# Optimization experiments

Measured on AMD Instinct MI355X. Metric: run time of the kernel, lower is better.

The kernel has to match this reference:

```python
import jax, jax.numpy as jnp
import numpy as np

N_MEL = 80; ENC = 512; ARNN = 1024; DRNN = 1024; PRE = 256
ADIM = 128; NFILT = 32; KS = 31
B = 16; T_ENC = 128; T_DEC = 128
NEG = -1e30  # stand-in for -inf mask value


def _lstm_cell(x, h, c, wih, whh, bih, bhh):
    # PyTorch LSTMCell gate order: i, f, g, o
    gates = x @ wih.T + h @ whh.T + bih + bhh
    i, f, g, o = jnp.split(gates, 4, axis=-1)
    c = jax.nn.sigmoid(f) * c + jax.nn.sigmoid(i) * jnp.tanh(g)
    h = jax.nn.sigmoid(o) * jnp.tanh(c)
    return h, c


def _forward(memory, mels, memory_lengths, prenet_w1, prenet_w2,
             arnn_wih, arnn_whh, arnn_bih, arnn_bhh,
             query_w, memory_w, v_w, loc_conv_w, loc_dense_w,
             drnn_wih, drnn_whh, drnn_bih, drnn_bhh,
             proj_w, proj_b, gate_w, gate_b):
    bsz, t_enc, enc = memory.shape
    t_dec = mels.shape[2]
    valid = jnp.arange(t_enc)[None, :] < memory_lengths[:, None]  # [B,T_enc]
    proc_mem = memory @ memory_w.T  # [B,T_enc,ADIM], precomputed once

    # parse_decoder_inputs + go frame: use go frame + teacher frames 0..T-2
    teacher = jnp.transpose(mels, (2, 0, 1))  # [T_dec,B,n_mel]
    go = jnp.zeros((1, bsz, mels.shape[1]), mels.dtype)
    dec_in = jnp.concatenate([go, teacher], axis=0)[:t_dec]
    # Prenet (dropout is p=0.0 in source, so omitted)
    x = jax.nn.relu(dec_in @ prenet_w1.T)
    x = jax.nn.relu(x @ prenet_w2.T)  # [T_dec,B,PRE]

    pad = (KS - 1) // 2

    def step(carry, x_t):
        attn_h, attn_c, dec_h, dec_c, aw, awc, ctx = carry
        # attention RNN
        cell_in = jnp.concatenate([x_t, ctx], axis=-1)
        attn_h2, attn_c2 = _lstm_cell(cell_in, attn_h, attn_c,
                                      arnn_wih, arnn_whh, arnn_bih, arnn_bhh)
        # location-sensitive attention
        aw_cat = jnp.stack([aw, awc], axis=1)  # [B,2,T_enc]
        loc = jax.lax.conv_general_dilated(
            aw_cat, loc_conv_w, (1,), [(pad, pad)],
            dimension_numbers=('NCH', 'OIH', 'NCH'))  # [B,NFILT,T_enc]
        loc = jnp.einsum('bft,af->bta', loc, loc_dense_w)  # [B,T_enc,ADIM]
        pq = attn_h2 @ query_w.T  # [B,ADIM]
        e = jnp.tanh(pq[:, None, :] + loc + proc_mem) @ v_w[0]  # [B,T_enc]
        e = jnp.where(valid, e, NEG)
        aw2 = jax.nn.softmax(e, axis=1)
        ctx2 = jnp.einsum('bt,bte->be', aw2, memory)  # [B,ENC]
        awc2 = awc + aw2
        # decoder RNN
        dec_in2 = jnp.concatenate([attn_h2, ctx2], axis=-1)
        dec_h2, dec_c2 = _lstm_cell(dec_in2, dec_h, dec_c,
                                    drnn_wih, drnn_whh, drnn_bih, drnn_bhh)
        hc = jnp.concatenate([dec_h2, ctx2], axis=-1)
        mel = hc @ proj_w.T + proj_b      # [B,n_mel]
        gate = hc @ gate_w.T + gate_b     # [B,1]
        new_carry = (attn_h2, attn_c2, dec_h2, dec_c2, aw2, awc2, ctx2)
        return new_carry, (mel, gate[:, 0], aw2)

    z = lambda *s: jnp.zeros(s, memory.dtype)
    carry0 = (z(bsz, ARNN), z(bsz, ARNN), z(bsz, DRNN), z(bsz, DRNN),
              z(bsz, t_enc), z(bsz, t_enc), z(bsz, enc))
    _, (mels_out, gates, aligns) = jax.lax.scan(step, carry0, x)
    mel_outputs = jnp.transpose(mels_out, (1, 2, 0))   # [B,n_mel,T_dec]
    gate_outputs = jnp.transpose(gates, (1, 0))        # [B,T_dec]
    alignments = jnp.transpose(aligns, (1, 0, 2))      # [B,T_dec,T_enc]
    return mel_outputs, gate_outputs, alignments


def setup_inputs() -> dict:
    key = jax.random.key(0)
    ks = jax.random.split(key, 24)

    def g(i, shape):
        fan_in = shape[-1] if len(shape) <= 2 else int(np.prod(shape[1:]))
        return jax.random.normal(ks[i], shape, jnp.float32) / np.float32(np.sqrt(fan_in))

    return {
        'memory': jax.random.normal(ks[0], (B, T_ENC, ENC), jnp.float32),
        'mels': jax.random.normal(ks[1], (B, N_MEL, T_DEC), jnp.float32),
        'memory_lengths': jax.random.randint(ks[2], (B,), T_ENC // 2, T_ENC + 1),
        'prenet_w1': g(3, (PRE, N_MEL)),
        'prenet_w2': g(4, (PRE, PRE)),
        'arnn_wih': g(5, (4 * ARNN, PRE + ENC)),
        'arnn_whh': g(6, (4 * ARNN, ARNN)),
        'arnn_bih': g(7, (4 * ARNN,)),
        'arnn_bhh': g(8, (4 * ARNN,)),
        'query_w': g(9, (ADIM, ARNN)),
        'memory_w': g(10, (ADIM, ENC)),
        'v_w': g(11, (1, ADIM)),
        'loc_conv_w': g(12, (NFILT, 2, KS)),
        'loc_dense_w': g(13, (ADIM, NFILT)),
        'drnn_wih': g(14, (4 * DRNN, ARNN + ENC)),
        'drnn_whh': g(15, (4 * DRNN, DRNN)),
        'drnn_bih': g(16, (4 * DRNN,)),
        'drnn_bhh': g(17, (4 * DRNN,)),
        'proj_w': g(18, (N_MEL, DRNN + ENC)),
        'proj_b': g(19, (N_MEL,)),
        'gate_w': g(20, (1, DRNN + ENC)),
        'gate_b': g(21, (1,)),
    }


def reference(memory, mels, memory_lengths, prenet_w1, prenet_w2,
              arnn_wih, arnn_whh, arnn_bih, arnn_bhh,
              query_w, memory_w, v_w, loc_conv_w, loc_dense_w,
              drnn_wih, drnn_whh, drnn_bih, drnn_bhh,
              proj_w, proj_b, gate_w, gate_b):
    return _forward(memory, mels, memory_lengths, prenet_w1, prenet_w2,
                    arnn_wih, arnn_whh, arnn_bih, arnn_bhh,
                    query_w, memory_w, v_w, loc_conv_w, loc_dense_w,
                    drnn_wih, drnn_whh, drnn_bih, drnn_bhh,
                    proj_w, proj_b, gate_w, gate_b)
```

## Files before the change

kernel.cpp:

```cpp
#include <hip/hip_runtime.h>
#include <hip/hip_cooperative_groups.h>

namespace cg = cooperative_groups;

#define N_MEL 80
#define ENC   512
#define ARNN  1024
#define PRE   256
#define ADIM  128
#define NFILT 32
#define KS    31
#define BSZ   16
#define TENC  128
#define TDEC  128

#define OFF_XA     0u
#define OFF_X      8388608u
#define OFF_H1     8912896u
#define OFF_DECIN  9437184u
#define OFF_PM     9601024u
#define OFF_ATTNH  9863168u
#define OFF_DECH   9895936u
#define OFF_CTX    9928704u
#define OFF_CTR    9945088u
#define STATE_FLOATS 82496

typedef float vf4 __attribute__((ext_vector_type(4)));

__device__ __forceinline__ float sigmf(float x) { return 1.0f / (1.0f + __expf(-x)); }
__device__ __forceinline__ float tanhfast(float x) { return 1.0f - 2.0f / (__expf(2.0f * x) + 1.0f); }
__device__ __forceinline__ float dot4(const float4& w, const vf4& x) {
    return w.x * x.x + w.y * x.y + w.z * x.z + w.w * x.w;
}
__device__ __forceinline__ float dot4f(const float4& w, const float4& x) {
    return w.x * x.x + w.y * x.y + w.z * x.z + w.w * x.w;
}

__device__ __forceinline__ vf4 vload4(const float* p) { return *(const volatile vf4*)p; }
__device__ __forceinline__ float vloadf(const float* p) { return *(const volatile float*)p; }
__device__ __forceinline__ void vstoref(float* p, float v) { *(volatile float*)p = v; }

__device__ __forceinline__ void wait_ge(unsigned* p, unsigned tgt) {
    while (__hip_atomic_load(p, __ATOMIC_RELAXED, __HIP_MEMORY_SCOPE_AGENT) < tgt)
        __builtin_amdgcn_s_sleep(1);
    asm volatile("" ::: "memory");
}


__global__ void __launch_bounds__(1024) build_decin(const float* __restrict__ mels,
                                                    float* __restrict__ decin) {
    int idx = blockIdx.x * 1024 + threadIdx.x;
    if (idx >= 128 * 16 * 80) return;
    int t = idx / 1280, r = idx % 1280;
    int b = r / 80, m = r % 80;
    decin[idx] = (t == 0) ? 0.f : mels[b * (80 * 128) + m * 128 + (t - 1)];
}

__global__ void __launch_bounds__(256) gemm_kernel(
    const float* __restrict__ A, int lda,
    const float* __restrict__ B, int ldb,
    float* __restrict__ C, int ldc,
    int M, int N, int K,
    const float* __restrict__ bias1, const float* __restrict__ bias2, int relu) {
    __shared__ float As[16][68];
    __shared__ float Bs[16][68];
    int tid = threadIdx.x;
    int tn = tid & 15, tm = tid >> 4;
    int m0 = blockIdx.y * 64, n0 = blockIdx.x * 64;
    float acc[4][4] = {};
    for (int k0 = 0; k0 < K; k0 += 16) {
        for (int idx = tid; idx < 1024; idx += 256) {
            int mm = idx >> 4, kk = idx & 15;
            int kg = k0 + kk;
            As[kk][mm] = (kg < K) ? A[(size_t)(m0 + mm) * lda + kg] : 0.f;
            Bs[kk][mm] = (kg < K) ? B[(size_t)(n0 + mm) * ldb + kg] : 0.f;
        }
        __syncthreads();
#pragma unroll
        for (int kk = 0; kk < 16; kk++) {
            float av[4], bv[4];
#pragma unroll
            for (int i = 0; i < 4; i++) { av[i] = As[kk][tm * 4 + i]; bv[i] = Bs[kk][tn * 4 + i]; }
#pragma unroll
            for (int i = 0; i < 4; i++)
#pragma unroll
                for (int j = 0; j < 4; j++) acc[i][j] += av[i] * bv[j];
        }
        __syncthreads();
    }
    for (int i = 0; i < 4; i++) {
        int m = m0 + tm * 4 + i;
        for (int j = 0; j < 4; j++) {
            int n = n0 + tn * 4 + j;
            float v = acc[i][j];
            if (bias1) v += bias1[n];
            if (bias2) v += bias2[n];
            if (relu) v = fmaxf(v, 0.f);
            C[(size_t)m * ldc + n] = v;
        }
    }
}


struct DecArgs {
    const float* memory;
    const int* memlen;
    const float* arnn_wih;
    const float* arnn_whh;
    const float* drnn_wih;
    const float* drnn_whh;
    const float* drnn_bih;
    const float* drnn_bhh;
    const float* query_w;
    const float* v_w;
    const float* conv_w;
    const float* dense_w;
    const float* proj_w;
    const float* proj_b;
    const float* gate_w;
    const float* gate_b;
    float* ws;
    float* out;
};

__global__ void __launch_bounds__(512, 2) decoder_main(DecArgs A) {
    cg::grid_group grid = cg::this_grid();
    const int tid = threadIdx.x;
    const int wv = tid >> 6;
    const int l = tid & 63;
    const int blk = blockIdx.x;
    const int u = wv & 3;
    const int kq = wv >> 2;
    const int jj = blk * 4 + u;
    const int col = kq * 256 + l * 4;
    float* ws = A.ws;
    unsigned* ctrA = (unsigned*)(ws + OFF_CTR);
    unsigned* ctrB = (unsigned*)(ws + OFF_CTR + 32);
    const int grp = blk >> 4;
    unsigned* subA = (unsigned*)(ws + OFF_CTR + 64 + grp * 32);

    __shared__ float s_pm[128 * 132];
    __shared__ float s_loc[128 * 33];
    __shared__ float s_dw[128 * 33];
    __shared__ float s_cw[1984];
    __shared__ float s_ah[1024];
    __shared__ float s_ep[512];
    __shared__ float s_part[8][64];
    __shared__ float s_pp[8][64];
    __shared__ float s_pq[128];
    __shared__ float s_aw2[128];
    __shared__ float s_awl[128];
    __shared__ float s_awcl[128];
    __shared__ float s_attnc[64];
    __shared__ float s_decc[64];
    __shared__ float s_db[16];
    __shared__ float s_vw[128];
    __shared__ float s_red[2];

    {
        int g = blk * 512 + tid;
        if (g < STATE_FLOATS) ws[OFF_ATTNH + g] = 0.f;
    }
    if (tid < 128) { s_awl[tid] = 0.f; s_awcl[tid] = 0.f; }
    if (tid < 64) { s_attnc[tid] = 0.f; s_decc[tid] = 0.f; }
    if (tid < 16) {
        int uu = tid >> 2, gg = tid & 3;
        s_db[tid] = A.drnn_bih[gg * 1024 + blk * 4 + uu] + A.drnn_bhh[gg * 1024 + blk * 4 + uu];
    }
    if (tid < 128) s_vw[tid] = A.v_w[tid];
    for (int idx = tid; idx < 4096; idx += 512) {
        int a = idx >> 5, f = idx & 31;
        s_dw[a * 33 + f] = A.dense_w[idx];
    }
    if (blk < 16) {
        for (int idx = tid; idx < 16384; idx += 512) {
            int tt = idx >> 7, a = idx & 127;
            s_pm[tt * 132 + a] = ws[OFF_PM + (blk * 128 + tt) * 128 + a];
        }
        for (int idx = tid; idx < 1984; idx += 512) s_cw[idx] = A.conv_w[idx];
    }
    const int ml = (blk < 16) ? A.memlen[blk] : 0;

    float4 wA[12];
    {
#pragma unroll
        for (int g = 0; g < 4; g++)
            wA[g] = *reinterpret_cast<const float4*>(
                A.arnn_wih + (size_t)(g * 1024 + jj) * 768 + 256 + col);
#pragma unroll
        for (int ch = 1; ch < 3; ch++)
#pragma unroll
            for (int g = 0; g < 4; g++)
                wA[ch * 4 + g] = *reinterpret_cast<const float4*>(
                    A.arnn_whh + (size_t)(g * 1024 + jj) * 1024 + (ch - 1) * 512 + col);
    }
    float4 wD[20];
    {
#pragma unroll
        for (int ch = 0; ch < 3; ch++)
#pragma unroll
            for (int g = 0; g < 4; g++)
                wD[ch * 4 + g] = *reinterpret_cast<const float4*>(
                    A.drnn_wih + (size_t)(g * 1024 + jj) * 1536 + ch * 512 + col);
#pragma unroll
        for (int ch = 3; ch < 5; ch++)
#pragma unroll
            for (int g = 0; g < 4; g++)
                wD[ch * 4 + g] = *reinterpret_cast<const float4*>(
                    A.drnn_whh + (size_t)(g * 1024 + jj) * 1024 + (ch - 3) * 512 + col);
    }
    __syncthreads();
    grid.sync();

    auto reduce4 = [&](float p0, float p1, float p2, float p3) -> float {
        float a01 = (l & 1) ? p1 : p0;
        float b01 = (l & 1) ? p0 : p1;
        a01 += __shfl_xor(b01, 1);
        float a23 = (l & 1) ? p3 : p2;
        float b23 = (l & 1) ? p2 : p3;
        a23 += __shfl_xor(b23, 1);
        float k_ = (l & 2) ? a23 : a01;
        float s_ = (l & 2) ? a01 : a23;
        k_ += __shfl_xor(s_, 2);
        k_ += __shfl_xor(k_, 4);
        k_ += __shfl_xor(k_, 8);
        k_ += __shfl_xor(k_, 16);
        k_ += __shfl_xor(k_, 32);
        return k_;
    };

    auto attn_stage = [&](int t, int wpar, int rpar) {
        const float* hb = ws + OFF_ATTNH + rpar * 16384;
        const float* cb = ws + OFF_CTX + rpar * 8192;
        float xa0 = 0.f, xa1 = 0.f, xa2 = 0.f, xa3 = 0.f;
        if (tid < 64) {
            int eb = tid & 15, eu = tid >> 4;
            const float* xa = ws + OFF_XA + (size_t)(t * 16 + eb) * 4096 + (blk * 4 + eu);
            xa0 = xa[0]; xa1 = xa[1024]; xa2 = xa[2048]; xa3 = xa[3072];
        }
#pragma unroll 4
        for (int b = 0; b < 16; b++) {
            vf4 x0 = vload4(cb + b * 512 + col);
            vf4 x1 = vload4(hb + b * 1024 + col);
            vf4 x2 = vload4(hb + b * 1024 + 512 + col);
            float p0 = dot4(wA[0], x0) + dot4(wA[4], x1) + dot4(wA[8], x2);
            float p1 = dot4(wA[1], x0) + dot4(wA[5], x1) + dot4(wA[9], x2);
            float p2 = dot4(wA[2], x0) + dot4(wA[6], x1) + dot4(wA[10], x2);
            float p3 = dot4(wA[3], x0) + dot4(wA[7], x1) + dot4(wA[11], x2);
            float r = reduce4(p0, p1, p2, p3);
            if (l < 4) s_part[wv][b * 4 + l] = r;
        }
        __syncthreads();
        if (tid < 64) {
            int eu = tid >> 4, eb = tid & 15;
            float G0 = s_part[eu][eb * 4 + 0] + s_part[eu + 4][eb * 4 + 0] + xa0;
            float G1 = s_part[eu][eb * 4 + 1] + s_part[eu + 4][eb * 4 + 1] + xa1;
            float G2 = s_part[eu][eb * 4 + 2] + s_part[eu + 4][eb * 4 + 2] + xa2;
            float G3 = s_part[eu][eb * 4 + 3] + s_part[eu + 4][eb * 4 + 3] + xa3;
            float ig = sigmf(G0), fg = sigmf(G1), gg = tanhfast(G2), og = sigmf(G3);
            float c = fg * s_attnc[tid] + ig * gg;
            s_attnc[tid] = c;
            vstoref(ws + OFF_ATTNH + wpar * 16384 + eb * 1024 + blk * 4 + eu, og * tanhfast(c));
        }
    };

    auto dec_partial = [&](int wpar, int rpar) {
        const float* hb = ws + OFF_ATTNH + wpar * 16384;
        const float* db = ws + OFF_DECH + rpar * 16384;
#pragma unroll 2
        for (int b = 0; b < 16; b++) {
            vf4 x0 = vload4(hb + b * 1024 + col);
            vf4 x1 = vload4(hb + b * 1024 + 512 + col);
            vf4 x3 = vload4(db + b * 1024 + col);
            vf4 x4 = vload4(db + b * 1024 + 512 + col);
            float p0 = dot4(wD[0], x0) + dot4(wD[4], x1) + dot4(wD[12], x3) + dot4(wD[16], x4);
            float p1 = dot4(wD[1], x0) + dot4(wD[5], x1) + dot4(wD[13], x3) + dot4(wD[17], x4);
            float p2 = dot4(wD[2], x0) + dot4(wD[6], x1) + dot4(wD[14], x3) + dot4(wD[18], x4);
            float p3 = dot4(wD[3], x0) + dot4(wD[7], x1) + dot4(wD[15], x3) + dot4(wD[19], x4);
            float r = reduce4(p0, p1, p2, p3);
            if (l < 4) s_pp[wv][b * 4 + l] = r;
        }
    };

    auto dec_tail = [&](int wpar) {
        const float* cb = ws + OFF_CTX + wpar * 8192;
#pragma unroll 4
        for (int b = 0; b < 16; b++) {
            vf4 x2 = vload4(cb + b * 512 + col);
            float p0 = dot4(wD[8], x2);
            float p1 = dot4(wD[9], x2);
            float p2 = dot4(wD[10], x2);
            float p3 = dot4(wD[11], x2);
            float r = reduce4(p0, p1, p2, p3);
            if (l < 4) s_part[wv][b * 4 + l] = r;
        }
        __syncthreads();
        if (tid < 64) {
            int eu = tid >> 4, eb = tid & 15;
            float G0 = s_part[eu][eb * 4 + 0] + s_part[eu + 4][eb * 4 + 0]
                     + s_pp[eu][eb * 4 + 0] + s_pp[eu + 4][eb * 4 + 0] + s_db[eu * 4 + 0];
            float G1 = s_part[eu][eb * 4 + 1] + s_part[eu + 4][eb * 4 + 1]
                     + s_pp[eu][eb * 4 + 1] + s_pp[eu + 4][eb * 4 + 1] + s_db[eu * 4 + 1];
            float G2 = s_part[eu][eb * 4 + 2] + s_part[eu + 4][eb * 4 + 2]
                     + s_pp[eu][eb * 4 + 2] + s_pp[eu + 4][eb * 4 + 2] + s_db[eu * 4 + 2];
            float G3 = s_part[eu][eb * 4 + 3] + s_part[eu + 4][eb * 4 + 3]
                     + s_pp[eu][eb * 4 + 3] + s_pp[eu + 4][eb * 4 + 3] + s_db[eu * 4 + 3];
            float ig = sigmf(G0), fg = sigmf(G1), gg = tanhfast(G2), og = sigmf(G3);
            float c = fg * s_decc[tid] + ig * gg;
            s_decc[tid] = c;
            vstoref(ws + OFF_DECH + wpar * 16384 + eb * 1024 + blk * 4 + eu, og * tanhfast(c));
        }
        __syncthreads();
    };

    auto attention = [&](int t, int wpar) {
        const int b = blk;
        s_ah[tid] = vloadf(ws + OFF_ATTNH + wpar * 16384 + b * 1024 + tid);
        s_ah[tid + 512] = vloadf(ws + OFF_ATTNH + wpar * 16384 + b * 1024 + 512 + tid);
        for (int idx = tid; idx < 4096; idx += 512) {
            int f = idx >> 7, tt = idx & 127;
            const float* w0 = s_cw + f * 62;
            float s = 0.f;
#pragma unroll
            for (int k = 0; k < 31; k++) {
                int j = tt + k - 15;
                if (j >= 0 && j < 128) s += w0[k] * s_awl[j] + w0[31 + k] * s_awcl[j];
            }
            s_loc[tt * 33 + f] = s;
        }
        __syncthreads();
#pragma unroll 4
        for (int ii = 0; ii < 16; ii++) {
            int a = wv * 16 + ii;
            const float* qw = A.query_w + a * 1024;
            float s = 0.f;
#pragma unroll
            for (int q = 0; q < 4; q++) {
                int k = q * 256 + l * 4;
                float4 h4 = *reinterpret_cast<const float4*>(&s_ah[k]);
                float4 w4 = *reinterpret_cast<const float4*>(&qw[k]);
                s += dot4f(w4, h4);
            }
#pragma unroll
            for (int off = 1; off < 64; off <<= 1) s += __shfl_xor(s, off);
            if (l == 0) s_pq[a] = s;
        }
        __syncthreads();
        {
            int tt = tid >> 2, sl = tid & 3;
            float part = 0.f;
            for (int i = 0; i < 32; i++) {
                int a = i * 4 + sl;
                float lp = 0.f;
#pragma unroll
                for (int f = 0; f < 32; f++) lp += s_loc[tt * 33 + f] * s_dw[a * 33 + f];
                float arg = s_pq[a] + lp + s_pm[tt * 132 + a];
                part += s_vw[a] * tanhfast(arg);
            }
            s_ep[tid] = part;
        }
        __syncthreads();
        if (tid < 128) {
            float s = s_ep[tid * 4] + s_ep[tid * 4 + 1] + s_ep[tid * 4 + 2] + s_ep[tid * 4 + 3];
            s_aw2[tid] = (tid >= ml) ? 0.f : __expf(s);
        }
        __syncthreads();
        if (wv == 0) {
            float s = s_aw2[l] + s_aw2[l + 64];
#pragma unroll
            for (int off = 1; off < 64; off <<= 1) s += __shfl_xor(s, off);
            if (l == 0) s_red[0] = 1.f / s;
        }
        __syncthreads();
        if (tid < 128) {
            float val = s_aw2[tid] * s_red[0];
            s_aw2[tid] = val;
            s_awl[tid] = val;
            s_awcl[tid] += val;
            A.out[165888 + b * 16384 + t * 128 + tid] = val;
        }
        __syncthreads();
        {
            const float* mb = A.memory + (size_t)b * 65536 + tid;
            float acc = 0.f;
#pragma unroll 8
            for (int tt2 = 0; tt2 < 128; tt2++) acc += s_aw2[tt2] * mb[tt2 * 512];
            vstoref(ws + OFF_CTX + wpar * 8192 + b * 512 + tid, acc);
        }
    };

    auto eout = [&](int tdone) {
        int widx = (blk - 16) * 8 + wv;
        if (widx >= 1296) return;
        int ppar = tdone & 1;
        int b; const float* wrow; float bias; float* dst;
        if (widx < 1280) {
            b = widx / 80; int m = widx % 80;
            wrow = A.proj_w + m * 1536; bias = A.proj_b[m];
            dst = A.out + (size_t)(b * 80 + m) * 128 + tdone;
        } else {
            b = widx - 1280;
            wrow = A.gate_w; bias = A.gate_b[0];
            dst = A.out + 163840 + b * 128 + tdone;
        }
        const float* h1p = ws + OFF_DECH + ppar * 16384 + b * 1024;
        const float* c1p = ws + OFF_CTX + ppar * 8192 + b * 512;
        float s = 0.f;
#pragma unroll
        for (int q = 0; q < 6; q++) {
            int k = q * 256 + l * 4;
            float4 w4 = *reinterpret_cast<const float4*>(&wrow[k]);
            vf4 h4;
            if (k < 1024) h4 = vload4(h1p + k);
            else h4 = vload4(c1p + k - 1024);
            s += dot4(w4, h4);
        }
#pragma unroll
        for (int off = 1; off < 64; off <<= 1) s += __shfl_xor(s, off);
        if (l == 0) *dst = s + bias;
    };

    for (int t = 0; t < 128; t++) {
        int wpar = t & 1, rpar = wpar ^ 1;
        attn_stage(t, wpar, rpar);
        __syncthreads();
        if (tid == 0) {
            asm volatile("s_waitcnt vmcnt(0)" ::: "memory");
            unsigned old = __hip_atomic_fetch_add(subA, 1u, __ATOMIC_RELAXED,
                                                  __HIP_MEMORY_SCOPE_AGENT);
            if (old == 16u * (unsigned)(t + 1) - 1u)
                __hip_atomic_fetch_add(ctrA, 1u, __ATOMIC_RELAXED,
                                       __HIP_MEMORY_SCOPE_AGENT);
        }
        if (blk < 16) {
            if (tid == 0) wait_ge(ctrA, 16u * (unsigned)(t + 1));
            __syncthreads();
            attention(t, wpar);
            __syncthreads();
            if (tid == 0) {
                asm volatile("s_waitcnt vmcnt(0)" ::: "memory");
                __hip_atomic_fetch_add(ctrB, 1u, __ATOMIC_RELAXED,
                                       __HIP_MEMORY_SCOPE_AGENT);
            }
            dec_partial(wpar, rpar);
            if (tid == 0) wait_ge(ctrB, 16u * (unsigned)(t + 1));
            __syncthreads();
            dec_tail(wpar);
        } else {
            if (tid == 0) wait_ge(ctrA, 16u * (unsigned)(t + 1));
            __syncthreads();
            if (t >= 1) eout(t - 1);
            dec_partial(wpar, rpar);
            if (tid == 0) wait_ge(ctrB, 16u * (unsigned)(t + 1));
            __syncthreads();
            dec_tail(wpar);
        }
    }
    if (tid == 0) {
        asm volatile("s_waitcnt vmcnt(0)" ::: "memory");
        unsigned old = __hip_atomic_fetch_add(subA, 1u, __ATOMIC_RELAXED,
                                              __HIP_MEMORY_SCOPE_AGENT);
        if (old == 16u * 129u - 1u)
            __hip_atomic_fetch_add(ctrA, 1u, __ATOMIC_RELAXED, __HIP_MEMORY_SCOPE_AGENT);
    }
    if (blk >= 16) {
        if (tid == 0) wait_ge(ctrA, 16u * 129u);
        __syncthreads();
        eout(127);
    }
}


extern "C" void kernel_launch(void* const* d_in, const int* in_sizes, int n_in,
                              void* d_out, int out_size, void* d_ws, size_t ws_size,
                              hipStream_t stream) {
    (void)in_sizes; (void)n_in; (void)out_size; (void)ws_size;
    const float* memory    = (const float*)d_in[0];
    const float* mels      = (const float*)d_in[1];
    const int*   memlen    = (const int*)d_in[2];
    const float* prenet_w1 = (const float*)d_in[3];
    const float* prenet_w2 = (const float*)d_in[4];
    const float* arnn_wih  = (const float*)d_in[5];
    const float* arnn_whh  = (const float*)d_in[6];
    const float* arnn_bih  = (const float*)d_in[7];
    const float* arnn_bhh  = (const float*)d_in[8];
    const float* query_w   = (const float*)d_in[9];
    const float* memory_w  = (const float*)d_in[10];
    const float* v_w       = (const float*)d_in[11];
    const float* conv_w    = (const float*)d_in[12];
    const float* dense_w   = (const float*)d_in[13];
    const float* drnn_wih  = (const float*)d_in[14];
    const float* drnn_whh  = (const float*)d_in[15];
    const float* drnn_bih  = (const float*)d_in[16];
    const float* drnn_bhh  = (const float*)d_in[17];
    const float* proj_w    = (const float*)d_in[18];
    const float* proj_b    = (const float*)d_in[19];
    const float* gate_w    = (const float*)d_in[20];
    const float* gate_b    = (const float*)d_in[21];
    float* ws = (float*)d_ws;
    float* out = (float*)d_out;

    build_decin<<<dim3(160), dim3(1024), 0, stream>>>(mels, ws + OFF_DECIN);
    gemm_kernel<<<dim3(4, 32), dim3(256), 0, stream>>>(ws + OFF_DECIN, 80, prenet_w1, 80,
                                                       ws + OFF_H1, 256, 2048, 256, 80,
                                                       nullptr, nullptr, 1);
    gemm_kernel<<<dim3(4, 32), dim3(256), 0, stream>>>(ws + OFF_H1, 256, prenet_w2, 256,
                                                       ws + OFF_X, 256, 2048, 256, 256,
                                                       nullptr, nullptr, 1);
    gemm_kernel<<<dim3(64, 32), dim3(256), 0, stream>>>(ws + OFF_X, 256, arnn_wih, 768,
                                                        ws + OFF_XA, 4096, 2048, 4096, 256,
                                                        arnn_bih, arnn_bhh, 0);
    gemm_kernel<<<dim3(2, 32), dim3(256), 0, stream>>>(memory, 512, memory_w, 512,
                                                       ws + OFF_PM, 128, 2048, 128, 512,
                                                       nullptr, nullptr, 0);

    DecArgs a;
    a.memory = memory; a.memlen = memlen;
    a.arnn_wih = arnn_wih; a.arnn_whh = arnn_whh;
    a.drnn_wih = drnn_wih; a.drnn_whh = drnn_whh;
    a.drnn_bih = drnn_bih; a.drnn_bhh = drnn_bhh;
    a.query_w = query_w; a.v_w = v_w;
    a.conv_w = conv_w; a.dense_w = dense_w;
    a.proj_w = proj_w; a.proj_b = proj_b;
    a.gate_w = gate_w; a.gate_b = gate_b;
    a.ws = ws; a.out = out;
    void* kargs[] = { &a };
    hipLaunchCooperativeKernel((const void*)decoder_main, dim3(256), dim3(512),
                               kargs, 0, stream);
}
```

Baseline: 12.00 ms.

## Hierarchical barrier broadcast with LDS spin and overlapped location conv

Attention blocks now post barrier completion to per-group broadcast flags, so the other blocks spin on a group-local global word instead of all polling the same counters. Inside each block, the non-leader waves spin on an LDS flag while doing dummy FMA work, which keeps them busy rather than idling at the barrier. The location convolution is moved ahead of the attention-stage wait so it overlaps the global barrier. This adds more synchronization state, and the busy spinning could compete with the leader thread or affect clock behaviour.

```diff
diff --git a/kernel.cpp b/kernel.cpp
--- a/kernel.cpp
+++ b/kernel.cpp
@@ -23,7 +23,7 @@
 #define OFF_DECH   9895936u
 #define OFF_CTX    9928704u
 #define OFF_CTR    9945088u
-#define STATE_FLOATS 82496
+#define STATE_FLOATS 83520
 
 typedef float vf4 __attribute__((ext_vector_type(4)));
 
@@ -45,6 +45,25 @@
         __builtin_amdgcn_s_sleep(1);
     asm volatile("" ::: "memory");
 }
+
+#define LDS_SPIN(idx, tgt)                                                      \
+    do {                                                                        \
+        float j0_ = 1.f, j1_ = 1.f;                                             \
+        while (__hip_atomic_load(&s_done[idx], __ATOMIC_RELAXED,                \
+                                 __HIP_MEMORY_SCOPE_WORKGROUP) < (tgt)) {       \
+            _Pragma("unroll")                                                   \
+            for (int i_ = 0; i_ < 32; i_++) {                                   \
+                j0_ = __builtin_fmaf(j0_, 1.0000001f, 1e-30f);                  \
+                j1_ = __builtin_fmaf(j1_, 0.9999999f, 1e-30f);                  \
+            }                                                                   \
+        }                                                                       \
+        asm volatile("" :: "v"(j0_), "v"(j1_));                                 \
+        asm volatile("" ::: "memory");                                          \
+    } while (0)
+
+#define LDS_POST(idx, val)                                                      \
+    __hip_atomic_store(&s_done[idx], (int)(val), __ATOMIC_RELAXED,              \
+                       __HIP_MEMORY_SCOPE_WORKGROUP)
 
 
 __global__ void __launch_bounds__(1024) build_decin(const float* __restrict__ mels,
@@ -137,7 +156,9 @@
     unsigned* ctrA = (unsigned*)(ws + OFF_CTR);
     unsigned* ctrB = (unsigned*)(ws + OFF_CTR + 32);
     const int grp = blk >> 4;
-    unsigned* subA = (unsigned*)(ws + OFF_CTR + 64 + grp * 32);
+    unsigned* subA   = (unsigned*)(ws + OFF_CTR + 64 + grp * 32);
+    unsigned* bcastA = (unsigned*)(ws + OFF_CTR + 576);
+    unsigned* bcastB = (unsigned*)(ws + OFF_CTR + 1088);
 
     __shared__ float s_pm[128 * 132];
     __shared__ float s_loc[128 * 33];
@@ -156,11 +177,13 @@
     __shared__ float s_db[16];
     __shared__ float s_vw[128];
     __shared__ float s_red[2];
+    __shared__ int   s_done[2];
 
     {
         int g = blk * 512 + tid;
         if (g < STATE_FLOATS) ws[OFF_ATTNH + g] = 0.f;
     }
+    if (tid < 2) s_done[tid] = 0;
     if (tid < 128) { s_awl[tid] = 0.f; s_awcl[tid] = 0.f; }
     if (tid < 64) { s_attnc[tid] = 0.f; s_decc[tid] = 0.f; }
     if (tid < 16) {
@@ -313,10 +336,7 @@
         __syncthreads();
     };
 
-    auto attention = [&](int t, int wpar) {
-        const int b = blk;
-        s_ah[tid] = vloadf(ws + OFF_ATTNH + wpar * 16384 + b * 1024 + tid);
-        s_ah[tid + 512] = vloadf(ws + OFF_ATTNH + wpar * 16384 + b * 1024 + 512 + tid);
+    auto loc_conv = [&]() {
         for (int idx = tid; idx < 4096; idx += 512) {
             int f = idx >> 7, tt = idx & 127;
             const float* w0 = s_cw + f * 62;
@@ -328,6 +348,12 @@
             }
             s_loc[tt * 33 + f] = s;
         }
+    };
+
+    auto attention_rest = [&](int t, int wpar) {
+        const int b = blk;
+        s_ah[tid] = vloadf(ws + OFF_ATTNH + wpar * 16384 + b * 1024 + tid);
+        s_ah[tid + 512] = vloadf(ws + OFF_ATTNH + wpar * 16384 + b * 1024 + 512 + tid);
         __syncthreads();
 #pragma unroll 4
         for (int ii = 0; ii < 16; ii++) {
@@ -422,20 +448,28 @@
 
     for (int t = 0; t < 128; t++) {
         int wpar = t & 1, rpar = wpar ^ 1;
+        unsigned tg = (unsigned)(t + 1);
         attn_stage(t, wpar, rpar);
         __syncthreads();
         if (tid == 0) {
             asm volatile("s_waitcnt vmcnt(0)" ::: "memory");
             unsigned old = __hip_atomic_fetch_add(subA, 1u, __ATOMIC_RELAXED,
                                                   __HIP_MEMORY_SCOPE_AGENT);
-            if (old == 16u * (unsigned)(t + 1) - 1u)
+            if (old == 16u * tg - 1u)
                 __hip_atomic_fetch_add(ctrA, 1u, __ATOMIC_RELAXED,
                                        __HIP_MEMORY_SCOPE_AGENT);
         }
         if (blk < 16) {
-            if (tid == 0) wait_ge(ctrA, 16u * (unsigned)(t + 1));
+            loc_conv();
             __syncthreads();
-            attention(t, wpar);
+            if (tid == 0) {
+                wait_ge(ctrA, 16u * tg);
+                __hip_atomic_store(bcastA + blk * 8, tg, __ATOMIC_RELAXED,
+                                   __HIP_MEMORY_SCOPE_AGENT);
+                LDS_POST(0, tg);
+            } else if (wv > 0) LDS_SPIN(0, (int)tg);
+            __syncthreads();
+            attention_rest(t, wpar);
             __syncthreads();
             if (tid == 0) {
                 asm volatile("s_waitcnt vmcnt(0)" ::: "memory");
@@ -443,15 +477,26 @@
                                        __HIP_MEMORY_SCOPE_AGENT);
             }
             dec_partial(wpar, rpar);
-            if (tid == 0) wait_ge(ctrB, 16u * (unsigned)(t + 1));
+            if (tid == 0) {
+                wait_ge(ctrB, 16u * tg);
+                __hip_atomic_store(bcastB + blk * 8, tg, __ATOMIC_RELAXED,
+                                   __HIP_MEMORY_SCOPE_AGENT);
+                LDS_POST(1, tg);
+            } else if (wv > 0) LDS_SPIN(1, (int)tg);
             __syncthreads();
             dec_tail(wpar);
         } else {
-            if (tid == 0) wait_ge(ctrA, 16u * (unsigned)(t + 1));
+            if (tid == 0) {
+                wait_ge(bcastA + grp * 8, tg);
+                LDS_POST(0, tg);
+            } else if (wv > 0) LDS_SPIN(0, (int)tg);
             __syncthreads();
             if (t >= 1) eout(t - 1);
             dec_partial(wpar, rpar);
-            if (tid == 0) wait_ge(ctrB, 16u * (unsigned)(t + 1));
+            if (tid == 0) {
+                wait_ge(bcastB + grp * 8, tg);
+                LDS_POST(1, tg);
+            } else if (wv > 0) LDS_SPIN(1, (int)tg);
             __syncthreads();
             dec_tail(wpar);
         }
@@ -463,8 +508,15 @@
         if (old == 16u * 129u - 1u)
             __hip_atomic_fetch_add(ctrA, 1u, __ATOMIC_RELAXED, __HIP_MEMORY_SCOPE_AGENT);
     }
-    if (blk >= 16) {
-        if (tid == 0) wait_ge(ctrA, 16u * 129u);
+    if (blk < 16) {
+        if (tid == 0) {
+            wait_ge(ctrA, 16u * 129u);
+            __hip_atomic_store(bcastA + blk * 8, 129u, __ATOMIC_RELAXED,
+                               __HIP_MEMORY_SCOPE_AGENT);
+        }
+    } else {
+        if (tid == 0) { wait_ge(bcastA + grp * 8, 129u); LDS_POST(0, 129); }
+        else if (wv > 0) LDS_SPIN(0, 129);
         __syncthreads();
         eout(127);
     }
```

New measurement: 11.94 ms. Within noise of the previous version (-0.5%).
